# Performance work log

Measured on AMD Instinct MI355X. Metric: run time of the kernel, lower is better.

## Reference

```python
import jax, jax.numpy as jnp
import numpy as np

N = 25000        # nodes
E = 400000       # edges (avg 16 neighbors)
C1 = 8           # output_size (scalar channels into TP)
COUT = 16        # channels_out
LMAX = 2
NB = 8           # number_of_basis
RMAX = 5.0       # max_radius
EMB = 16         # atom embedding dim
NATOM = 10
WNUM = (LMAX + 1) * C1 * COUT                 # per-edge TP weights (parity-shared, k0 paths)
TOTAL_DIM = 2 * COUT * (1 + 3 + 9)            # both parities x ranks 0..2 -> 416


def setup_inputs() -> dict:
    key = jax.random.key(0)
    ks = jax.random.split(key, 12)
    rn = lambda i, shape, s=1.0: jax.random.normal(ks[i], shape, jnp.float32) * s
    pos = rn(0, (N, 3)) * 3.0
    A = jax.random.randint(ks[1], (N,), 0, NATOM)
    batch = jnp.zeros((N,), jnp.int32)                       # single graph
    edge_src = jax.random.randint(ks[2], (E,), 0, N)
    # avoid self-edges (zero-length vectors)
    edge_dst = (edge_src + jax.random.randint(ks[3], (E,), 1, N)) % N
    edge_shifts = jnp.zeros((E, 3), jnp.float32)
    cell = jnp.eye(3, dtype=jnp.float32)[None] * 10.0        # [1,3,3]
    emb_table = rn(4, (NATOM, EMB))
    atom_w1 = rn(5, (EMB, 64), EMB ** -0.5)
    atom_b1 = jnp.zeros((64,), jnp.float32)
    atom_w2 = rn(6, (64, C1), 64 ** -0.5)
    atom_b2 = jnp.zeros((C1,), jnp.float32)
    fc_w1 = rn(7, (NB, 64), NB ** -0.5)
    fc_b1 = jnp.zeros((64,), jnp.float32)
    fc_w2 = rn(8, (64, 64), 64 ** -0.5)
    fc_b2 = jnp.zeros((64,), jnp.float32)
    fc_w3 = rn(9, (64, WNUM), 64 ** -0.5)
    fc_b3 = jnp.zeros((WNUM,), jnp.float32)
    return dict(pos=pos, A=A, batch=batch, edge_src=edge_src, edge_dst=edge_dst,
                edge_shifts=edge_shifts, cell=cell, emb_table=emb_table,
                atom_w1=atom_w1, atom_b1=atom_b1, atom_w2=atom_w2, atom_b2=atom_b2,
                fc_w1=fc_w1, fc_b1=fc_b1, fc_w2=fc_w2, fc_b2=fc_b2, fc_w3=fc_w3, fc_b3=fc_b3)


def reference(pos, A, batch, edge_src, edge_dst, edge_shifts, cell, emb_table,
              atom_w1, atom_b1, atom_w2, atom_b2,
              fc_w1, fc_b1, fc_w2, fc_b2, fc_w3, fc_b3):
    num_edges = edge_src.shape[0]
    num_nodes = pos.shape[0]
    # edge geometry (PBC shift)
    edge_cells = cell[batch[edge_src]]                                   # [E,3,3]
    shift_vecs = jnp.einsum('ni,nij->nj', edge_shifts, edge_cells)
    edge_vec = pos[edge_dst] - pos[edge_src] + shift_vecs                # [E,3]
    edge_length = jnp.sqrt(jnp.sum(edge_vec * edge_vec, axis=1) + 1e-12)
    # per-node scalar features -> gathered to edges
    Ai = jax.nn.silu(emb_table[A] @ atom_w1 + atom_b1) @ atom_w2 + atom_b2  # [N,C1]
    Ai_e = Ai[edge_src]                                                    # [E,C1]
    # edge_rank_powers (normalized): rank-0 scalar 1, rank-1 u, rank-2 u\otimes u
    u = edge_vec / edge_length[:, None]
    # radial basis: e3nn soft_one_hot_linspace (gaussian, cutoff) * sqrt(NB)
    values = jnp.linspace(0.0, RMAX, NB + 2)[1:-1]
    step = RMAX / (NB + 1)
    diff = (edge_length[:, None] - values) / step
    emb = (jnp.exp(-diff * diff) / 1.12) * (NB ** 0.5)                     # [E,NB]
    # radial MLP -> per-edge TP weights
    h = jax.nn.silu(emb @ fc_w1 + fc_b1)
    h = jax.nn.silu(h @ fc_w2 + fc_b2)
    w = (h @ fc_w3 + fc_b3).reshape(num_edges, LMAX + 1, C1, COUT)
    # sparse cartesian O(3) tensor product (k0 paths; only (0,0)x(0,L)->(0,L) nonzero
    # since all x1 L>=1 and parity-1 blocks are zero by construction)
    b0 = jnp.einsum('eco,ec->eo', w[:, 0], Ai_e)                           # [E,COUT]
    b1 = jnp.einsum('eco,ec,ei->eoi', w[:, 1], Ai_e, u)                    # [E,COUT,3]
    b2 = jnp.einsum('eco,ec,ei,ej->eoij', w[:, 2], Ai_e, u, u)             # [E,COUT,3,3]
    feats = jnp.concatenate([b0, b1.reshape(num_edges, -1), b2.reshape(num_edges, -1)], axis=1)
    edge_features = jnp.concatenate([feats, jnp.zeros_like(feats)], axis=1)  # pseudo blocks = 0
    # scatter-sum to destination nodes, normalize by global avg num neighbors
    out = jax.ops.segment_sum(edge_features, edge_dst, num_segments=num_nodes)
    avg_num_neighbors = jnp.maximum(jnp.float32(num_edges) / jnp.float32(num_nodes), 1e-8)
    return out / avg_num_neighbors
```

## Files before the change

### kernel.cpp

```cpp
#include <hip/hip_runtime.h>
#include <math.h>

#define NN 25000
#define NE 400000
#define TD 416
#define TCAP 46080
#define NROWS (TCAP * 10)
#define PLH 64
#define GROWS 32

typedef __attribute__((ext_vector_type(8))) __bf16 bf16x8;
typedef __attribute__((ext_vector_type(4))) _Float16 f16x4;
typedef __attribute__((ext_vector_type(4))) float f32x4;

__device__ __forceinline__ float silu_f(float x) {
    return x * __builtin_amdgcn_rcpf(1.0f + __expf(-x));
}

__global__ __launch_bounds__(256) void prep_count_k(
    const float* __restrict__ emb_table,
    const float* __restrict__ aw1, const float* __restrict__ ab1,
    const float* __restrict__ aw2, const float* __restrict__ ab2,
    const float* __restrict__ fw1, const float* __restrict__ fb1,
    const float* __restrict__ fw2,
    const float* __restrict__ fw3, const float* __restrict__ fb3,
    __bf16* __restrict__ w1a, __bf16* __restrict__ w2a,
    __bf16* __restrict__ w3ta, float* __restrict__ b3t,
    const int* __restrict__ esrc, const int* __restrict__ edst,
    const int* __restrict__ A,
    int* __restrict__ cnt_dst, int* __restrict__ cnt_t,
    int* __restrict__ rdst, int* __restrict__ rtp) {
    const int tid = threadIdx.x;
    if (blockIdx.x < 64) {
        __shared__ float s_ai[80];
        if (tid < 10) {
            float acc[8];
#pragma unroll
            for (int o = 0; o < 8; ++o) acc[o] = ab2[o];
            for (int j = 0; j < 64; ++j) {
                float h = ab1[j];
#pragma unroll
                for (int i = 0; i < 16; ++i) h += emb_table[tid * 16 + i] * aw1[i * 64 + j];
                h = silu_f(h);
#pragma unroll
                for (int o = 0; o < 8; ++o) acc[o] += h * aw2[j * 8 + o];
            }
#pragma unroll
            for (int o = 0; o < 8; ++o) s_ai[tid * 8 + o] = acc[o];
        }
        __syncthreads();
        for (int i = blockIdx.x * 256 + tid; i < 37344; i += 64 * 256) {
            if (i < 2048) {
                int m = i >> 9, r = i & 511, lane = r >> 3, j = r & 7;
                int k = (lane >> 4) * 8 + j, ch = m * 16 + (lane & 15);
                float v = (k < 8) ? fw1[k * 64 + ch] : ((k == 8) ? fb1[ch] : 0.0f);
                w1a[i] = (__bf16)v;
            } else if (i < 6144) {
                int q = i - 2048;
                int mk = q >> 9, lane = (q >> 3) & 63, j = q & 7;
                int m = mk >> 1, kt = mk & 1;
                int k = kt * 32 + (lane >> 4) * 8 + j, ch = m * 16 + (lane & 15);
                w2a[q] = (__bf16)fw2[k * 64 + ch];
            } else if (i < 36864) {
                int q = i - 6144;
                int tmk = q >> 9, lane = (q >> 3) & 63, j = q & 7;
                int kt = tmk & 1, tm = tmk >> 1;
                int t = tm / 3, m = tm - t * 3;
                int k = kt * 32 + (lane >> 4) * 8 + j, ch = m * 16 + (lane & 15);
                int l = ch >> 4, o = ch & 15;
                float s = 0.f;
#pragma unroll
                for (int c = 0; c < 8; ++c)
                    s += s_ai[t * 8 + c] * fw3[k * 384 + l * 128 + c * 16 + o];
                w3ta[q] = (__bf16)s;
            } else {
                int q2 = i - 36864;
                int t = q2 / 48, ch = q2 - t * 48;
                int l = ch >> 4, o = ch & 15;
                float s = 0.f;
#pragma unroll
                for (int c = 0; c < 8; ++c)
                    s += s_ai[t * 8 + c] * fb3[l * 128 + c * 16 + o];
                b3t[q2] = s;
            }
        }
    } else {
        __shared__ int lcnt[10];
        __shared__ int gbase[10];
        if (tid < 10) lcnt[tid] = 0;
        __syncthreads();
        int e = (blockIdx.x - 64) * 256 + tid;
        int t = 0, lr = 0;
        bool valid = e < NE;
        if (valid) {
            rdst[e] = atomicAdd(&cnt_dst[edst[e]], 1);
            t = A[esrc[e]];
            lr = atomicAdd(&lcnt[t], 1);
        }
        __syncthreads();
        if (tid < 10) gbase[tid] = atomicAdd(&cnt_t[tid], lcnt[tid]);
        __syncthreads();
        if (valid) rtp[e] = (t << 20) | (gbase[t] + lr);
    }
}

__global__ __launch_bounds__(256) void alloc_k(const int* __restrict__ cnt_dst,
                                               int* __restrict__ off_dst,
                                               int* __restrict__ bump) {
    __shared__ int s[256];
    __shared__ int sbase;
    const int tid = threadIdx.x;
    const int idx = blockIdx.x * 256 + tid;
    int c = (idx < NN) ? cnt_dst[idx] : 0;
    s[tid] = c;
    __syncthreads();
    for (int off = 1; off < 256; off <<= 1) {
        int v = (tid >= off) ? s[tid - off] : 0;
        __syncthreads();
        s[tid] += v;
        __syncthreads();
    }
    if (tid == 255) sbase = atomicAdd(bump, s[255]);
    __syncthreads();
    if (idx < NN) off_dst[idx] = sbase + s[tid] - c;
}

__global__ void scatter_k(const int* __restrict__ edst,
                          const int* __restrict__ off_dst,
                          const int* __restrict__ rdst, const int* __restrict__ rtp,
                          int* __restrict__ elist, int* __restrict__ tlist) {
    int e = blockIdx.x * blockDim.x + threadIdx.x;
    if (e >= NE) return;
    int rp = rtp[e];
    int p = (rp >> 20) * TCAP + (rp & 0xFFFFF);
    tlist[p] = e;
    elist[off_dst[edst[e]] + rdst[e]] = p;
}

__global__ __launch_bounds__(64, 4) void edge_k(
    const int* __restrict__ tlist, const int* __restrict__ A,
    const int* __restrict__ esrc, const int* __restrict__ edst,
    const float* __restrict__ pos, const float* __restrict__ shifts,
    const float* __restrict__ cell, const int* __restrict__ batch,
    const __bf16* __restrict__ w1a, const __bf16* __restrict__ w2a,
    const __bf16* __restrict__ w3ta,
    const float* __restrict__ fb2, const float* __restrict__ b3t,
    _Float16* __restrict__ payload) {
    __shared__ __bf16 embuf[64 * 36];
    __shared__ __bf16 h1buf[16 * 72];
    __shared__ __bf16 h2buf[16 * 72];
    const int lane = threadIdx.x;
    const int base = blockIdx.x * 64;
    const int e0 = tlist[base];
    if (e0 < 0) return;
    int t_blk = __builtin_amdgcn_readfirstlane(A[esrc[e0]]);

    int eid = tlist[base + lane];
    if (eid < 0) eid = e0;

    const int src = esrc[eid], dstn = edst[eid];
    const int b = batch[src];
    const float* cb = cell + b * 9;
    const float sh0 = shifts[eid * 3 + 0], sh1 = shifts[eid * 3 + 1], sh2 = shifts[eid * 3 + 2];
    float vx = pos[dstn * 3 + 0] - pos[src * 3 + 0] + sh0 * cb[0] + sh1 * cb[3] + sh2 * cb[6];
    float vy = pos[dstn * 3 + 1] - pos[src * 3 + 1] + sh0 * cb[1] + sh1 * cb[4] + sh2 * cb[7];
    float vz = pos[dstn * 3 + 2] - pos[src * 3 + 2] + sh0 * cb[2] + sh1 * cb[5] + sh2 * cb[8];
    const float l2 = vx * vx + vy * vy + vz * vz + 1e-12f;
    const float il = __builtin_amdgcn_rsqf(l2);
    const float len = l2 * il;
    {
        union { float f[4]; uint4 u; } uu;
        uu.f[0] = vx * il; uu.f[1] = vy * il; uu.f[2] = vz * il; uu.f[3] = 0.f;
        *(uint4*)(payload + (size_t)(base + lane) * PLH + 48) = uu.u;
    }

    bf16x8 er0;
#pragma unroll
    for (int k = 0; k < 8; ++k) {
        float d = (len - (5.0f * (float)(k + 1) / 9.0f)) * 1.8f;
        er0[k] = (__bf16)(__expf(-d * d) * 2.525381361380528f);
    }
    bf16x8 er1 = {};
    er1[0] = (__bf16)1.0f;
    bf16x8 zz = {};
    *(bf16x8*)&embuf[lane * 36 + 0]  = er0;
    *(bf16x8*)&embuf[lane * 36 + 8]  = er1;
    *(bf16x8*)&embuf[lane * 36 + 16] = zz;
    *(bf16x8*)&embuf[lane * 36 + 24] = zz;

    bf16x8 a1[4], a2[8], a3[6];
#pragma unroll
    for (int m = 0; m < 4; ++m) a1[m] = *(const bf16x8*)(w1a + (m * 64 + lane) * 8);
#pragma unroll
    for (int i = 0; i < 8; ++i) a2[i] = *(const bf16x8*)(w2a + (i * 64 + lane) * 8);
#pragma unroll
    for (int i = 0; i < 6; ++i)
        a3[i] = *(const bf16x8*)(w3ta + ((size_t)(t_blk * 6 + i) * 64 + lane) * 8);
    const int qr = (lane >> 4) * 4;
    const int q8 = (lane >> 4) * 8;
    f32x4 bias2[4], bias3[3];
#pragma unroll
    for (int m = 0; m < 4; ++m) bias2[m] = *(const f32x4*)(fb2 + m * 16 + qr);
#pragma unroll
    for (int m = 0; m < 3; ++m) bias3[m] = *(const f32x4*)(b3t + t_blk * 48 + m * 16 + qr);
    __syncthreads();

    const float SC = (float)NN / (float)NE;
    const int colrow = lane & 15;
#pragma unroll 1
    for (int n = 0; n < 4; ++n) {
        const int erow = n * 16 + colrow;
        bf16x8 b1 = *(bf16x8*)&embuf[erow * 36 + q8];
#pragma unroll
        for (int m = 0; m < 4; ++m) {
            f32x4 c = {0.f, 0.f, 0.f, 0.f};
            c = __builtin_amdgcn_mfma_f32_16x16x32_bf16(a1[m], b1, c, 0, 0, 0);
            __bf16 hp[4];
#pragma unroll
            for (int r = 0; r < 4; ++r) hp[r] = (__bf16)silu_f(c[r]);
            *(uint2*)&h1buf[colrow * 72 + m * 16 + qr] = *(uint2*)hp;
        }
        __syncthreads();
        bf16x8 b20 = *(bf16x8*)&h1buf[colrow * 72 + q8];
        bf16x8 b21 = *(bf16x8*)&h1buf[colrow * 72 + 32 + q8];
#pragma unroll
        for (int m = 0; m < 4; ++m) {
            f32x4 c = bias2[m];
            c = __builtin_amdgcn_mfma_f32_16x16x32_bf16(a2[m * 2 + 0], b20, c, 0, 0, 0);
            c = __builtin_amdgcn_mfma_f32_16x16x32_bf16(a2[m * 2 + 1], b21, c, 0, 0, 0);
            __bf16 hp[4];
#pragma unroll
            for (int r = 0; r < 4; ++r) hp[r] = (__bf16)silu_f(c[r]);
            *(uint2*)&h2buf[colrow * 72 + m * 16 + qr] = *(uint2*)hp;
        }
        __syncthreads();
        bf16x8 b30 = *(bf16x8*)&h2buf[colrow * 72 + q8];
        bf16x8 b31 = *(bf16x8*)&h2buf[colrow * 72 + 32 + q8];
#pragma unroll
        for (int m = 0; m < 3; ++m) {
            f32x4 c = bias3[m];
            c = __builtin_amdgcn_mfma_f32_16x16x32_bf16(a3[m * 2 + 0], b30, c, 0, 0, 0);
            c = __builtin_amdgcn_mfma_f32_16x16x32_bf16(a3[m * 2 + 1], b31, c, 0, 0, 0);
            f16x4 hp;
#pragma unroll
            for (int r = 0; r < 4; ++r) hp[r] = (_Float16)(c[r] * SC);
            *(f16x4*)(payload + (size_t)(base + erow) * PLH + m * 16 + qr) = hp;
        }
    }
}

__global__ __launch_bounds__(256) void gather_k(const int* __restrict__ off_dst,
                                                const int* __restrict__ cnt_dst,
                                                const int* __restrict__ elist,
                                                const _Float16* __restrict__ payload,
                                                float* __restrict__ out) {
    __shared__ int spid[GROWS];
    __shared__ __align__(16) _Float16 sp_s[GROWS][72];
    __shared__ float sfac[GROWS][16];
    const int n = blockIdx.x;
    const int tid = threadIdx.x;
    const int lo = off_dst[n];
    const int cnt = cnt_dst[n];
    int voff = 0, foff = 0;
    if (tid < 16) { voff = tid; foff = 0; }
    else if (tid < 64) { int q = tid - 16; voff = 16 + q / 3; foff = 1 + q % 3; }
    else if (tid < 208) { int q = tid - 64; voff = 32 + q / 9; foff = 4 + q % 9; }
    float acc = 0.f;
    for (int p0 = 0; p0 < cnt; p0 += GROWS) {
        const int m = min(GROWS, cnt - p0);
        if (tid < m) spid[tid] = elist[lo + p0 + tid];
        __syncthreads();
        if (tid < m * 8) {
            int r = tid >> 3, q = tid & 7;
            ((uint4*)&sp_s[r][0])[q] = ((const uint4*)(payload + (size_t)spid[r] * PLH))[q];
        }
        __syncthreads();
        for (int idx = tid; idx < m * 16; idx += 256) {
            int r = idx >> 4, f = idx & 15;
            if (f < 13) {
                const float* uf = (const float*)&sp_s[r][48];
                float v;
                if (f == 0) v = 1.0f;
                else if (f < 4) v = uf[f - 1];
                else { int g = f - 4; v = uf[g / 3] * uf[g % 3]; }
                sfac[r][f] = v;
            }
        }
        __syncthreads();
        if (tid < 208)
            for (int r = 0; r < m; ++r)
                acc += (float)sp_s[r][voff] * sfac[r][foff];
        __syncthreads();
    }
    if (tid < 208) {
        out[(size_t)n * TD + tid] = acc;
        out[(size_t)n * TD + 208 + tid] = 0.f;
    }
}

extern "C" void kernel_launch(void* const* d_in, const int* in_sizes, int n_in,
                              void* d_out, int out_size, void* d_ws, size_t ws_size,
                              hipStream_t stream) {
    const float* pos       = (const float*)d_in[0];
    const int*   A         = (const int*)d_in[1];
    const int*   batch     = (const int*)d_in[2];
    const int*   esrc      = (const int*)d_in[3];
    const int*   edst      = (const int*)d_in[4];
    const float* shifts    = (const float*)d_in[5];
    const float* cell      = (const float*)d_in[6];
    const float* emb_table = (const float*)d_in[7];
    const float* aw1       = (const float*)d_in[8];
    const float* ab1       = (const float*)d_in[9];
    const float* aw2       = (const float*)d_in[10];
    const float* ab2       = (const float*)d_in[11];
    const float* fw1       = (const float*)d_in[12];
    const float* fb1       = (const float*)d_in[13];
    const float* fw2       = (const float*)d_in[14];
    const float* fb2       = (const float*)d_in[15];
    const float* fw3       = (const float*)d_in[16];
    const float* fb3       = (const float*)d_in[17];
    float* out = (float*)d_out;

    char* base = (char*)d_ws;
    __bf16* w1a    = (__bf16*)(base + 0);
    __bf16* w2a    = (__bf16*)(base + 4096);
    __bf16* w3ta   = (__bf16*)(base + 12288);
    float*  b3t    = (float*)(base + 73728);
    int* cnt_dst   = (int*)(base + 75648);
    int* cnt_t     = (int*)(base + 175680);
    int* bump      = (int*)(base + 175744);
    int* off_dst   = (int*)(base + 175808);
    int* rdst      = (int*)(base + 275840);
    int* rtp       = (int*)(base + 1875840);
    int* elist     = (int*)(base + 3475840);
    int* tlist     = (int*)(base + 5075840);
    _Float16* payload = (_Float16*)(base + 6919168);

    hipMemsetAsync(cnt_dst, 0, 100160, stream);
    hipMemsetAsync(tlist, 0xFF, NROWS * 4, stream);
    prep_count_k<<<64 + (NE + 255) / 256, 256, 0, stream>>>(
        emb_table, aw1, ab1, aw2, ab2, fw1, fb1, fw2, fw3, fb3,
        w1a, w2a, w3ta, b3t, esrc, edst, A, cnt_dst, cnt_t, rdst, rtp);
    alloc_k<<<(NN + 255) / 256, 256, 0, stream>>>(cnt_dst, off_dst, bump);
    scatter_k<<<(NE + 255) / 256, 256, 0, stream>>>(edst, off_dst, rdst, rtp, elist, tlist);
    edge_k<<<NROWS / 64, 64, 0, stream>>>(tlist, A, esrc, edst, pos, shifts, cell, batch,
                                          w1a, w2a, w3ta, fb2, b3t, payload);
    gather_k<<<NN, 256, 0, stream>>>(off_dst, cnt_dst, elist, payload, out);
}
```

Before: 208.8 us.

## Write edge payload in destination-sorted order and drop the scatter kernel

```diff
diff --git a/kernel.cpp b/kernel.cpp
--- a/kernel.cpp
+++ b/kernel.cpp
@@ -29,7 +29,7 @@
     const int* __restrict__ esrc, const int* __restrict__ edst,
     const int* __restrict__ A,
     int* __restrict__ cnt_dst, int* __restrict__ cnt_t,
-    int* __restrict__ rdst, int* __restrict__ rtp) {
+    int* __restrict__ rdst, int* __restrict__ tlist) {
     const int tid = threadIdx.x;
     if (blockIdx.x < 64) {
         __shared__ float s_ai[80];
@@ -100,7 +100,7 @@
         __syncthreads();
         if (tid < 10) gbase[tid] = atomicAdd(&cnt_t[tid], lcnt[tid]);
         __syncthreads();
-        if (valid) rtp[e] = (t << 20) | (gbase[t] + lr);
+        if (valid) tlist[t * TCAP + gbase[t] + lr] = e;
     }
 }
 
@@ -125,18 +125,6 @@
     if (idx < NN) off_dst[idx] = sbase + s[tid] - c;
 }
 
-__global__ void scatter_k(const int* __restrict__ edst,
-                          const int* __restrict__ off_dst,
-                          const int* __restrict__ rdst, const int* __restrict__ rtp,
-                          int* __restrict__ elist, int* __restrict__ tlist) {
-    int e = blockIdx.x * blockDim.x + threadIdx.x;
-    if (e >= NE) return;
-    int rp = rtp[e];
-    int p = (rp >> 20) * TCAP + (rp & 0xFFFFF);
-    tlist[p] = e;
-    elist[off_dst[edst[e]] + rdst[e]] = p;
-}
-
 __global__ __launch_bounds__(64, 4) void edge_k(
     const int* __restrict__ tlist, const int* __restrict__ A,
     const int* __restrict__ esrc, const int* __restrict__ edst,
@@ -145,10 +133,12 @@
     const __bf16* __restrict__ w1a, const __bf16* __restrict__ w2a,
     const __bf16* __restrict__ w3ta,
     const float* __restrict__ fb2, const float* __restrict__ b3t,
+    const int* __restrict__ off_dst, const int* __restrict__ rdst,
     _Float16* __restrict__ payload) {
     __shared__ __bf16 embuf[64 * 36];
     __shared__ __bf16 h1buf[16 * 72];
     __shared__ __bf16 h2buf[16 * 72];
+    __shared__ int pbuf[64];
     const int lane = threadIdx.x;
     const int base = blockIdx.x * 64;
     const int e0 = tlist[base];
@@ -159,6 +149,8 @@
     if (eid < 0) eid = e0;
 
     const int src = esrc[eid], dstn = edst[eid];
+    const int pd = off_dst[dstn] + rdst[eid];
+    pbuf[lane] = pd;
     const int b = batch[src];
     const float* cb = cell + b * 9;
     const float sh0 = shifts[eid * 3 + 0], sh1 = shifts[eid * 3 + 1], sh2 = shifts[eid * 3 + 2];
@@ -171,7 +163,7 @@
     {
         union { float f[4]; uint4 u; } uu;
         uu.f[0] = vx * il; uu.f[1] = vy * il; uu.f[2] = vz * il; uu.f[3] = 0.f;
-        *(uint4*)(payload + (size_t)(base + lane) * PLH + 48) = uu.u;
+        *(uint4*)(payload + (size_t)pd * PLH + 48) = uu.u;
     }
 
     bf16x8 er0;
@@ -234,6 +226,7 @@
             *(uint2*)&h2buf[colrow * 72 + m * 16 + qr] = *(uint2*)hp;
         }
         __syncthreads();
+        const int prow = pbuf[erow];
         bf16x8 b30 = *(bf16x8*)&h2buf[colrow * 72 + q8];
         bf16x8 b31 = *(bf16x8*)&h2buf[colrow * 72 + 32 + q8];
 #pragma unroll
@@ -244,17 +237,15 @@
             f16x4 hp;
 #pragma unroll
             for (int r = 0; r < 4; ++r) hp[r] = (_Float16)(c[r] * SC);
-            *(f16x4*)(payload + (size_t)(base + erow) * PLH + m * 16 + qr) = hp;
+            *(f16x4*)(payload + (size_t)prow * PLH + m * 16 + qr) = hp;
         }
     }
 }
 
 __global__ __launch_bounds__(256) void gather_k(const int* __restrict__ off_dst,
                                                 const int* __restrict__ cnt_dst,
-                                                const int* __restrict__ elist,
                                                 const _Float16* __restrict__ payload,
                                                 float* __restrict__ out) {
-    __shared__ int spid[GROWS];
     __shared__ __align__(16) _Float16 sp_s[GROWS][72];
     __shared__ float sfac[GROWS][16];
     const int n = blockIdx.x;
@@ -268,11 +259,9 @@
     float acc = 0.f;
     for (int p0 = 0; p0 < cnt; p0 += GROWS) {
         const int m = min(GROWS, cnt - p0);
-        if (tid < m) spid[tid] = elist[lo + p0 + tid];
-        __syncthreads();
         if (tid < m * 8) {
             int r = tid >> 3, q = tid & 7;
-            ((uint4*)&sp_s[r][0])[q] = ((const uint4*)(payload + (size_t)spid[r] * PLH))[q];
+            ((uint4*)&sp_s[r][0])[q] = ((const uint4*)(payload + (size_t)(lo + p0 + r) * PLH))[q];
         }
         __syncthreads();
         for (int idx = tid; idx < m * 16; idx += 256) {
@@ -331,19 +320,16 @@
     int* bump      = (int*)(base + 175744);
     int* off_dst   = (int*)(base + 175808);
     int* rdst      = (int*)(base + 275840);
-    int* rtp       = (int*)(base + 1875840);
-    int* elist     = (int*)(base + 3475840);
-    int* tlist     = (int*)(base + 5075840);
-    _Float16* payload = (_Float16*)(base + 6919168);
+    int* tlist     = (int*)(base + 1875840);
+    _Float16* payload = (_Float16*)(base + 3719168);
 
     hipMemsetAsync(cnt_dst, 0, 100160, stream);
     hipMemsetAsync(tlist, 0xFF, NROWS * 4, stream);
     prep_count_k<<<64 + (NE + 255) / 256, 256, 0, stream>>>(
         emb_table, aw1, ab1, aw2, ab2, fw1, fb1, fw2, fw3, fb3,
-        w1a, w2a, w3ta, b3t, esrc, edst, A, cnt_dst, cnt_t, rdst, rtp);
+        w1a, w2a, w3ta, b3t, esrc, edst, A, cnt_dst, cnt_t, rdst, tlist);
     alloc_k<<<(NN + 255) / 256, 256, 0, stream>>>(cnt_dst, off_dst, bump);
-    scatter_k<<<(NE + 255) / 256, 256, 0, stream>>>(edst, off_dst, rdst, rtp, elist, tlist);
     edge_k<<<NROWS / 64, 64, 0, stream>>>(tlist, A, esrc, edst, pos, shifts, cell, batch,
-                                          w1a, w2a, w3ta, fb2, b3t, payload);
-    gather_k<<<NN, 256, 0, stream>>>(off_dst, cnt_dst, elist, payload, out);
-}
+                                          w1a, w2a, w3ta, fb2, b3t, off_dst, rdst, payload);
+    gather_k<<<NN, 256, 0, stream>>>(off_dst, cnt_dst, payload, out);
+}
```

Result: faster. 199.9 us (-4.3%).
